# Performance work log

Hardware: AMD Instinct MI355X
Metric: run time of the kernel (lower is better)

The kernel has to match this reference:

```python
import jax, jax.numpy as jnp
import numpy as np

B, L, D, F = 1, 4096, 4096, 11008
# (start, end, side): side 0 = vision expert, side 1 = language expert.
# Mirrors merge_section_size over alternating contiguous vision/language token ranges.
SEGMENTS = [(0, 1024, 0), (1024, 2048, 1), (2048, 3072, 0), (3072, 4096, 1)]


def setup_inputs() -> dict:
    key = jax.random.key(0)
    ks = jax.random.split(key, 7)
    s = 0.02  # weight init scale
    hidden_states = jax.random.normal(ks[0], (B, L, D), jnp.float32)
    tt = np.zeros((B, L), np.int32)
    for a, b, side in SEGMENTS:
        tt[:, a:b] = side
    token_type_ids = jnp.asarray(tt)
    lg_w = jax.random.normal(ks[1], (D, F), jnp.float32) * s
    lu_w = jax.random.normal(ks[2], (D, F), jnp.float32) * s
    ld_w = jax.random.normal(ks[3], (F, D), jnp.float32) * s
    vg_w = jax.random.normal(ks[4], (D, F), jnp.float32) * s
    vu_w = jax.random.normal(ks[5], (D, F), jnp.float32) * s
    vd_w = jax.random.normal(ks[6], (F, D), jnp.float32) * s
    return {
        'hidden_states': hidden_states,
        'token_type_ids': token_type_ids,
        'lg_w': lg_w, 'lu_w': lu_w, 'ld_w': ld_w,
        'vg_w': vg_w, 'vu_w': vu_w, 'vd_w': vd_w,
    }


def _swiglu_mlp(x, gw, uw, dw):
    # x: [B, T, D] -> [B, T, D]; down(silu(gate(x)) * up(x))
    h = jax.nn.silu(jnp.einsum('btd,df->btf', x, gw)) * jnp.einsum('btd,df->btf', x, uw)
    return jnp.einsum('btf,fd->btd', h, dw)


def reference(hidden_states, token_type_ids, lg_w, lu_w, ld_w, vg_w, vu_w, vd_w):
    # Split-dispatch over static contiguous segments, then concat along seq dim.
    outs = []
    for a, b, side in SEGMENTS:
        seg = hidden_states[:, a:b, :]
        if side == 1:
            outs.append(_swiglu_mlp(seg, lg_w, lu_w, ld_w))
        else:
            outs.append(_swiglu_mlp(seg, vg_w, vu_w, vd_w))
    return jnp.concatenate(outs, axis=1)
```

## Files before the change

kernel.cpp:

```cpp
#include <hip/hip_runtime.h>
#include <math.h>

typedef unsigned short u16;
typedef short s16x8 __attribute__((ext_vector_type(8)));
typedef float f32x4 __attribute__((ext_vector_type(4)));

#define GLOAD16(gp, lp)                                                        \
  __builtin_amdgcn_global_load_lds(                                            \
      (const __attribute__((address_space(1))) void*)(gp),                     \
      (__attribute__((address_space(3))) void*)(lp), 16, 0, 0)

__device__ __forceinline__ u16 f2bf(float f) {
  union { float f; unsigned u; } v; v.f = f;
  unsigned r = v.u + 0x7fffu + ((v.u >> 16) & 1u);
  return (u16)(r >> 16);
}

__global__ __launch_bounds__(256) void cvt_x_kernel(const float* __restrict__ in,
                                                    u16* __restrict__ out) {
  size_t i = ((size_t)blockIdx.x * 256 + threadIdx.x) * 8;
  float4 a = *(const float4*)(in + i);
  float4 b = *(const float4*)(in + i + 4);
  s16x8 v;
  v[0] = (short)f2bf(a.x); v[1] = (short)f2bf(a.y);
  v[2] = (short)f2bf(a.z); v[3] = (short)f2bf(a.w);
  v[4] = (short)f2bf(b.x); v[5] = (short)f2bf(b.y);
  v[6] = (short)f2bf(b.z); v[7] = (short)f2bf(b.w);
  *(s16x8*)(out + i) = v;
}

__global__ __launch_bounds__(256) void transpose_cvt_kernel(
    const float* __restrict__ in0, const float* __restrict__ in1,
    const float* __restrict__ in2, const float* __restrict__ in3,
    const float* __restrict__ in4, const float* __restrict__ in5,
    u16* __restrict__ o01, u16* __restrict__ o23,
    u16* __restrict__ o4, u16* __restrict__ o5) {
  __shared__ float s[64 * 65];
  const int mat = blockIdx.y;
  const float* in; u16* out;
  switch (mat) {
    case 0: in = in0; out = o01; break;
    case 1: in = in1; out = o01; break;
    case 2: in = in2; out = o23; break;
    case 3: in = in3; out = o23; break;
    case 4: in = in4; out = o4; break;
    default: in = in5; out = o5; break;
  }
  const int R = (mat < 4) ? 4096 : 11008;
  const int C = (mat < 4) ? 11008 : 4096;
  const int nTc = C >> 6;
  const int tr = blockIdx.x / nTc, tc = blockIdx.x - tr * nTc;
  const int r0 = tr << 6, c0 = tc << 6;
  const int t = threadIdx.x;
#pragma unroll
  for (int p = 0; p < 4; ++p) {
    const int lr = p * 16 + (t >> 4);
    const int lc = (t & 15) * 4;
    float4 v = *(const float4*)(in + (size_t)(r0 + lr) * C + (c0 + lc));
    float* sp = &s[lr * 65 + lc];
    sp[0] = v.x; sp[1] = v.y; sp[2] = v.z; sp[3] = v.w;
  }
  __syncthreads();
#pragma unroll
  for (int q = 0; q < 2; ++q) {
    const int oc = q * 32 + (t >> 3);
    const int orr = (t & 7) * 8;
    s16x8 v;
#pragma unroll
    for (int i = 0; i < 8; ++i) v[i] = (short)f2bf(s[(orr + i) * 65 + oc]);
    const int f = c0 + oc;
    size_t orow;
    if (mat < 4) orow = (size_t)((f >> 4) << 5) + ((mat & 1) << 4) + (f & 15);
    else         orow = (size_t)f;
    *(s16x8*)(out + orow * R + (r0 + orr)) = v;
  }
}

template <int KB, int EPI>
__global__ __launch_bounds__(512, 1) void gemm256(
    const u16* __restrict__ A, const u16* __restrict__ Bl,
    const u16* __restrict__ Bv, const int* __restrict__ tt,
    void* __restrict__ OutP) {
  constexpr int NK = KB / 128;
  constexpr int L = NK / 2;
  __shared__ u16 sA[2][2][128][64];
  __shared__ u16 sB[2][2][128][64];

  const int nwg = gridDim.x;
  const int bid = blockIdx.x;
  const int wg = (bid & 7) * (nwg >> 3) + (bid >> 3);
  const int mT = wg & 15;
  const int nT = wg >> 4;

  const int t = threadIdx.x;
  const int lane = t & 63;
  const int rlo = lane & 15;
  const int hi = lane >> 4;
  const int wn = (t >> 6) & 3;
  const int wm = (t >> 8) & 1;

  const int side = tt[mT << 8];
  const u16* B = side ? Bl : Bv;

  const int rowq = t >> 3;
  const int gsw = ((t & 7) ^ (rowq & 7)) << 4;
  const char* srcA = (const char*)A + (size_t)(mT * 256 + rowq) * KB + gsw;
  const char* srcB = (const char*)B + (size_t)(nT * 256 + rowq) * KB + gsw;
  char* ldsA = (char*)&sA[0][0][0][0];
  char* ldsB = (char*)&sB[0][0][0][0];
  const int woff = (t & 448) << 4;

#define STG_A(d, h, kt)                                                        \
  do {                                                                         \
    GLOAD16(srcA + (size_t)((h) * 128) * KB + (kt) * 128,                      \
            ldsA + (d) * 32768 + (h) * 16384 + woff);                          \
    GLOAD16(srcA + (size_t)((h) * 128 + 64) * KB + (kt) * 128,                 \
            ldsA + (d) * 32768 + (h) * 16384 + 8192 + woff);                   \
  } while (0)
#define STG_B(d, h, kt)                                                        \
  do {                                                                         \
    GLOAD16(srcB + (size_t)((h) * 128) * KB + (kt) * 128,                      \
            ldsB + (d) * 32768 + (h) * 16384 + woff);                          \
    GLOAD16(srcB + (size_t)((h) * 128 + 64) * KB + (kt) * 128,                 \
            ldsB + (d) * 32768 + (h) * 16384 + 8192 + woff);                   \
  } while (0)

  const int cxa = (hi ^ (rlo & 7)) << 4;
  const int cxb = ((4 + hi) ^ (rlo & 7)) << 4;
  const int arow = (wm * 64 + rlo) * 128;
  const int brow = (wn * 32 + rlo) * 128;

  s16x8 af[4][2], bf[2][2];
  f32x4 acc[8][4];
  const f32x4 z = {0.f, 0.f, 0.f, 0.f};
#pragma unroll
  for (int i = 0; i < 8; ++i)
#pragma unroll
    for (int j = 0; j < 4; ++j) acc[i][j] = z;

#define LDA(d, mh)                                                             \
  do {                                                                         \
    _Pragma("unroll") for (int fi = 0; fi < 4; ++fi) {                         \
      const char* p = ldsA + (d) * 32768 + (mh) * 16384 + arow + fi * 2048;    \
      af[fi][0] = *(const s16x8*)(p + cxa);                                    \
      af[fi][1] = *(const s16x8*)(p + cxb);                                    \
    }                                                                          \
  } while (0)
#define LDB(d, nh)                                                             \
  do {                                                                         \
    _Pragma("unroll") for (int gi = 0; gi < 2; ++gi) {                         \
      const char* p = ldsB + (d) * 32768 + (nh) * 16384 + brow + gi * 2048;    \
      bf[gi][0] = *(const s16x8*)(p + cxa);                                    \
      bf[gi][1] = *(const s16x8*)(p + cxb);                                    \
    }                                                                          \
  } while (0)
#define MFMA16(mh, nh)                                                         \
  do {                                                                         \
    __builtin_amdgcn_s_setprio(1);                                             \
    _Pragma("unroll") for (int fi = 0; fi < 4; ++fi)                           \
        _Pragma("unroll") for (int gi = 0; gi < 2; ++gi) {                     \
      acc[(mh)*4 + fi][(nh)*2 + gi] = __builtin_amdgcn_mfma_f32_16x16x32_bf16( \
          af[fi][0], bf[gi][0], acc[(mh)*4 + fi][(nh)*2 + gi], 0, 0, 0);       \
      acc[(mh)*4 + fi][(nh)*2 + gi] = __builtin_amdgcn_mfma_f32_16x16x32_bf16( \
          af[fi][1], bf[gi][1], acc[(mh)*4 + fi][(nh)*2 + gi], 0, 0, 0);       \
    }                                                                          \
    __builtin_amdgcn_s_setprio(0);                                             \
  } while (0)
#define SBAR() __builtin_amdgcn_s_barrier()
#define VMCNT4() do { asm volatile("s_waitcnt vmcnt(4)" ::: "memory");         \
                      __builtin_amdgcn_sched_barrier(0); } while (0)
#define VMCNT0() do { asm volatile("s_waitcnt vmcnt(0)" ::: "memory");         \
                      __builtin_amdgcn_sched_barrier(0); } while (0)

  STG_A(0, 0, 0); STG_A(0, 1, 0); STG_B(0, 0, 0); STG_B(0, 1, 0);
  STG_B(1, 0, 1); STG_A(1, 1, 1);
  VMCNT4();
  SBAR();

  for (int it = 0; it < L - 1; ++it) {
    const int T = 2 * it;
    LDA(0, 0); LDB(0, 0);
    STG_A(1, 0, T + 1); STG_B(1, 1, T + 1);
    SBAR(); MFMA16(0, 0); SBAR();
    LDA(0, 1);
    SBAR(); MFMA16(1, 0); SBAR();
    LDB(0, 1);
    STG_B(0, 0, T + 2);
    SBAR(); MFMA16(1, 1); SBAR();
    LDA(0, 0);
    STG_A(0, 1, T + 2);
    SBAR(); MFMA16(0, 1);
    VMCNT4(); SBAR();
    LDA(1, 0); LDB(1, 0);
    STG_A(0, 0, T + 2); STG_B(0, 1, T + 2);
    SBAR(); MFMA16(0, 0); SBAR();
    LDA(1, 1);
    SBAR(); MFMA16(1, 0); SBAR();
    LDB(1, 1);
    STG_B(1, 0, T + 3);
    SBAR(); MFMA16(1, 1); SBAR();
    LDA(1, 0);
    STG_A(1, 1, T + 3);
    SBAR(); MFMA16(0, 1);
    VMCNT4(); SBAR();
  }
  {
    const int T = NK - 2;
    LDA(0, 0); LDB(0, 0);
    STG_A(1, 0, T + 1); STG_B(1, 1, T + 1);
    SBAR(); MFMA16(0, 0); SBAR();
    LDA(0, 1);
    SBAR(); MFMA16(1, 0); SBAR();
    LDB(0, 1);
    SBAR(); MFMA16(1, 1); SBAR();
    LDA(0, 0);
    SBAR(); MFMA16(0, 1);
    VMCNT0(); SBAR();
    LDA(1, 0); LDB(1, 0);
    SBAR(); MFMA16(0, 0); SBAR();
    LDA(1, 1);
    SBAR(); MFMA16(1, 0); SBAR();
    LDB(1, 1);
    SBAR(); MFMA16(1, 1); SBAR();
    LDA(1, 0);
    SBAR(); MFMA16(0, 1);
  }

  if (EPI == 0) {
    u16* H = (u16*)OutP;
#pragma unroll
    for (int mh = 0; mh < 2; ++mh)
#pragma unroll
      for (int fi = 0; fi < 4; ++fi) {
        const int row0 = mT * 256 + mh * 128 + wm * 64 + fi * 16 + hi * 4;
#pragma unroll
        for (int nh = 0; nh < 2; ++nh) {
          const int fc = nT * 128 + (nh * 4 + wn) * 16 + rlo;
          const f32x4 g = acc[mh * 4 + fi][nh * 2 + 0];
          const f32x4 u = acc[mh * 4 + fi][nh * 2 + 1];
#pragma unroll
          for (int r = 0; r < 4; ++r) {
            const float gv = g[r];
            const float hv = gv / (1.f + __expf(-gv)) * u[r];
            H[(size_t)(row0 + r) * 11008 + fc] = f2bf(hv);
          }
        }
      }
  } else {
    float* O = (float*)OutP;
#pragma unroll
    for (int mh = 0; mh < 2; ++mh)
#pragma unroll
      for (int fi = 0; fi < 4; ++fi) {
        const int row0 = mT * 256 + mh * 128 + wm * 64 + fi * 16 + hi * 4;
#pragma unroll
        for (int nh = 0; nh < 2; ++nh)
#pragma unroll
          for (int gi = 0; gi < 2; ++gi) {
            const int col = nT * 256 + nh * 128 + wn * 32 + gi * 16 + rlo;
            const f32x4 a = acc[mh * 4 + fi][nh * 2 + gi];
#pragma unroll
            for (int r = 0; r < 4; ++r)
              O[(size_t)(row0 + r) * 4096 + col] = a[r];
          }
      }
  }
#undef STG_A
#undef STG_B
#undef LDA
#undef LDB
#undef MFMA16
#undef SBAR
#undef VMCNT4
#undef VMCNT0
}

extern "C" void kernel_launch(void* const* d_in, const int* in_sizes, int n_in,
                              void* d_out, int out_size, void* d_ws, size_t ws_size,
                              hipStream_t stream) {
  (void)in_sizes; (void)n_in; (void)out_size; (void)ws_size;
  const float* x  = (const float*)d_in[0];
  const int*   tt = (const int*)d_in[1];
  const float* lg = (const float*)d_in[2];
  const float* lu = (const float*)d_in[3];
  const float* ld = (const float*)d_in[4];
  const float* vg = (const float*)d_in[5];
  const float* vu = (const float*)d_in[6];
  const float* vd = (const float*)d_in[7];

  u16* ws  = (u16*)d_ws;
  u16* xbf = ws;
  u16* GUl = xbf + 16777216;
  u16* GUv = GUl + 90177536;
  u16* ldT = GUv + 90177536;
  u16* vdT = ldT + 45088768;
  u16* hbuf = vdT + 45088768;

  cvt_x_kernel<<<dim3(8192), dim3(256), 0, stream>>>(x, xbf);
  transpose_cvt_kernel<<<dim3(11008, 6), dim3(256), 0, stream>>>(
      lg, lu, vg, vu, ld, vd, GUl, GUv, ldT, vdT);
  gemm256<8192, 0><<<dim3(1376), dim3(512), 0, stream>>>(xbf, GUl, GUv, tt, hbuf);
  gemm256<22016, 1><<<dim3(256), dim3(512), 0, stream>>>(hbuf, ldT, vdT, tt, d_out);
}
```

Baseline: 1.520 ms.

## Switch GEMMs to 32x32 MFMA, persistent atomic tile queue, new gate/up interleave

Both GEMMs move from 16x16x32 to 32x32x16 bf16 MFMA with a new fragment layout and a simpler single-buffer-step pipeline that uses lgkmcnt waits in place of extra barriers. The gate/up weight interleave changes from 16-row to 128-row blocks to match the new accumulator tiling. The gate/up GEMM becomes a persistent 256-block kernel pulling tiles from an atomic counter, which is reset with a memset each call. The aim is fewer LDS reads per MFMA, fewer barriers and better load balance, at the cost of an added atomic per tile and more register pressure from the wider accumulators.

```diff
diff --git a/kernel.cpp b/kernel.cpp
--- a/kernel.cpp
+++ b/kernel.cpp
@@ -4,6 +4,7 @@
 typedef unsigned short u16;
 typedef short s16x8 __attribute__((ext_vector_type(8)));
 typedef float f32x4 __attribute__((ext_vector_type(4)));
+typedef float f32x16 __attribute__((ext_vector_type(16)));
 
 #define GLOAD16(gp, lp)                                                        \
   __builtin_amdgcn_global_load_lds(                                            \
@@ -70,209 +71,259 @@
     for (int i = 0; i < 8; ++i) v[i] = (short)f2bf(s[(orr + i) * 65 + oc]);
     const int f = c0 + oc;
     size_t orow;
-    if (mat < 4) orow = (size_t)((f >> 4) << 5) + ((mat & 1) << 4) + (f & 15);
+    if (mat < 4) orow = (size_t)((f >> 7) << 8) + ((mat & 1) << 7) + (f & 127);
     else         orow = (size_t)f;
     *(s16x8*)(out + orow * R + (r0 + orr)) = v;
   }
 }
 
-template <int KB, int EPI>
-__global__ __launch_bounds__(512, 1) void gemm256(
-    const u16* __restrict__ A, const u16* __restrict__ Bl,
-    const u16* __restrict__ Bv, const int* __restrict__ tt,
-    void* __restrict__ OutP) {
-  constexpr int NK = KB / 128;
-  constexpr int L = NK / 2;
+#define SBAR() __builtin_amdgcn_s_barrier()
+#define LGKM0() asm volatile("s_waitcnt lgkmcnt(0)")
+#define VMCNT4() asm volatile("s_waitcnt vmcnt(4)")
+#define VMCNT2() asm volatile("s_waitcnt vmcnt(2)")
+#define VMCNT0() asm volatile("s_waitcnt vmcnt(0)")
+
+#define LDA(d, mh)                                                             \
+  do {                                                                         \
+    _Pragma("unroll") for (int fj = 0; fj < 2; ++fj)                           \
+        _Pragma("unroll") for (int ks = 0; ks < 4; ++ks)                       \
+        af[fj][ks] = *(const s16x8*)(ldsA + (d) * 32768 + (mh) * 16384 +       \
+                                     arow + fj * 4096 + cx[ks]);               \
+  } while (0)
+#define LDB(d, nh)                                                             \
+  do {                                                                         \
+    _Pragma("unroll") for (int ks = 0; ks < 4; ++ks)                           \
+        bf[nh][ks] = *(const s16x8*)(ldsB + (d) * 32768 + (nh) * 16384 +       \
+                                     brow + cx[ks]);                           \
+  } while (0)
+#define MFMA8(mh, nh)                                                          \
+  do {                                                                         \
+    __builtin_amdgcn_s_setprio(1);                                             \
+    _Pragma("unroll") for (int fj = 0; fj < 2; ++fj)                           \
+        _Pragma("unroll") for (int ks = 0; ks < 4; ++ks)                       \
+        acc[mh][fj][nh] = __builtin_amdgcn_mfma_f32_32x32x16_bf16(             \
+            af[fj][ks], bf[nh][ks], acc[mh][fj][nh], 0, 0, 0);                 \
+    __builtin_amdgcn_s_setprio(0);                                             \
+  } while (0)
+
+#define STG_A(d, h, kt)                                                        \
+  do {                                                                         \
+    GLOAD16(srcA + (size_t)((h) * 128) * KB + (size_t)(kt) * 128,              \
+            ldsA + (d) * 32768 + (h) * 16384 + woff);                          \
+    GLOAD16(srcA + (size_t)((h) * 128 + 64) * KB + (size_t)(kt) * 128,         \
+            ldsA + (d) * 32768 + (h) * 16384 + 8192 + woff);                   \
+  } while (0)
+#define STG_B(d, h, kt)                                                        \
+  do {                                                                         \
+    GLOAD16(srcB + (size_t)((h) * 128) * KB + (size_t)(kt) * 128,              \
+            ldsB + (d) * 32768 + (h) * 16384 + woff);                          \
+    GLOAD16(srcB + (size_t)((h) * 128 + 64) * KB + (size_t)(kt) * 128,         \
+            ldsB + (d) * 32768 + (h) * 16384 + 8192 + woff);                   \
+  } while (0)
+
+__global__ __launch_bounds__(512, 1) void gemm_gateup_persist(
+    const u16* __restrict__ A, const u16* __restrict__ GUl,
+    const u16* __restrict__ GUv, const int* __restrict__ tt,
+    u16* __restrict__ H, int* __restrict__ qcnt) {
+  constexpr int KB = 8192;
+  constexpr int NKT = 64;
   __shared__ u16 sA[2][2][128][64];
   __shared__ u16 sB[2][2][128][64];
-
-  const int nwg = gridDim.x;
+  __shared__ int sQ;
+
+  const int t = threadIdx.x;
+  const int lane = t & 63;
+  const int l31 = lane & 31;
+  const int kg = lane >> 5;
+  const int wn = (t >> 6) & 3;
+  const int wm = (t >> 8) & 1;
+
+  const int rowq = t >> 3;
+  const int gsw = ((t & 7) ^ (rowq & 7)) << 4;
+  char* ldsA = (char*)&sA[0][0][0][0];
+  char* ldsB = (char*)&sB[0][0][0][0];
+  const int woff = (t & 448) << 4;
+
+  const int arow = (wm * 64 + l31) * 128;
+  const int brow = (wn * 32 + l31) * 128;
+  int cx[4];
+#pragma unroll
+  for (int ks = 0; ks < 4; ++ks) cx[ks] = ((2 * ks + kg) ^ (lane & 7)) << 4;
+
+  for (;;) {
+    __syncthreads();
+    if (t == 0) sQ = atomicAdd(qcnt, 1);
+    __syncthreads();
+    const int q = sQ;
+    if (q >= 1376) break;
+    const int nT = q >> 4;
+    const int mT = q & 15;
+    const int side = tt[mT << 8];
+    const u16* GU = side ? GUl : GUv;
+    const char* srcA = (const char*)A + (size_t)(mT * 256 + rowq) * KB + gsw;
+    const char* srcB = (const char*)GU + (size_t)(nT * 256 + rowq) * KB + gsw;
+
+    s16x8 af[2][4], bf[2][4];
+    f32x16 acc[2][2][2];
+#pragma unroll
+    for (int a = 0; a < 2; ++a)
+#pragma unroll
+      for (int b = 0; b < 2; ++b)
+#pragma unroll
+        for (int c = 0; c < 2; ++c)
+#pragma unroll
+          for (int r = 0; r < 16; ++r) acc[a][b][c][r] = 0.f;
+
+    STG_A(0, 0, 0); STG_B(0, 0, 0); STG_B(0, 1, 0); STG_A(0, 1, 0);
+    VMCNT4();
+    SBAR();
+
+    for (int T = 0; T < NKT - 1; ++T) {
+      const int d = T & 1, nd = d ^ 1;
+      LDA(d, 0); LDB(d, 0);
+      STG_A(nd, 0, T + 1);
+      LGKM0(); MFMA8(0, 0);
+      VMCNT4(); SBAR();
+      LDB(d, 1);
+      STG_B(nd, 0, T + 1);
+      LGKM0(); MFMA8(0, 1);
+      VMCNT4(); SBAR();
+      LDA(d, 1);
+      STG_B(nd, 1, T + 1);
+      LGKM0(); MFMA8(1, 1);
+      STG_A(nd, 1, T + 1);
+      MFMA8(1, 0);
+      VMCNT4(); SBAR();
+    }
+    {
+      const int d = (NKT - 1) & 1;
+      LDA(d, 0); LDB(d, 0);
+      LGKM0(); MFMA8(0, 0);
+      VMCNT2(); SBAR();
+      LDB(d, 1);
+      LGKM0(); MFMA8(0, 1);
+      VMCNT0(); SBAR();
+      LDA(d, 1);
+      LGKM0(); MFMA8(1, 1);
+      MFMA8(1, 0);
+    }
+
+    const int f = nT * 128 + wn * 32 + l31;
+#pragma unroll
+    for (int mh = 0; mh < 2; ++mh)
+#pragma unroll
+      for (int fj = 0; fj < 2; ++fj) {
+        const int rowbase = mT * 256 + mh * 128 + wm * 64 + fj * 32 + 4 * kg;
+#pragma unroll
+        for (int r = 0; r < 16; ++r) {
+          const int row = rowbase + (r & 3) + 8 * (r >> 2);
+          const float gv = acc[mh][fj][0][r];
+          const float uv = acc[mh][fj][1][r];
+          const float hv = gv / (1.f + __expf(-gv)) * uv;
+          H[(size_t)row * 11008 + f] = f2bf(hv);
+        }
+      }
+  }
+}
+
+__global__ __launch_bounds__(512, 1) void gemm_down(
+    const u16* __restrict__ Hm, const u16* __restrict__ Dl,
+    const u16* __restrict__ Dv, const int* __restrict__ tt,
+    float* __restrict__ O) {
+  constexpr int KB = 22016;
+  constexpr int NKT = 172;
+  __shared__ u16 sA[2][2][128][64];
+  __shared__ u16 sB[2][2][128][64];
+
   const int bid = blockIdx.x;
-  const int wg = (bid & 7) * (nwg >> 3) + (bid >> 3);
+  const int wg = (bid & 7) * 32 + (bid >> 3);
   const int mT = wg & 15;
   const int nT = wg >> 4;
 
   const int t = threadIdx.x;
   const int lane = t & 63;
-  const int rlo = lane & 15;
-  const int hi = lane >> 4;
+  const int l31 = lane & 31;
+  const int kg = lane >> 5;
   const int wn = (t >> 6) & 3;
   const int wm = (t >> 8) & 1;
 
   const int side = tt[mT << 8];
-  const u16* B = side ? Bl : Bv;
+  const u16* B = side ? Dl : Dv;
 
   const int rowq = t >> 3;
   const int gsw = ((t & 7) ^ (rowq & 7)) << 4;
-  const char* srcA = (const char*)A + (size_t)(mT * 256 + rowq) * KB + gsw;
+  const char* srcA = (const char*)Hm + (size_t)(mT * 256 + rowq) * KB + gsw;
   const char* srcB = (const char*)B + (size_t)(nT * 256 + rowq) * KB + gsw;
   char* ldsA = (char*)&sA[0][0][0][0];
   char* ldsB = (char*)&sB[0][0][0][0];
   const int woff = (t & 448) << 4;
 
-#define STG_A(d, h, kt)                                                        \
-  do {                                                                         \
-    GLOAD16(srcA + (size_t)((h) * 128) * KB + (kt) * 128,                      \
-            ldsA + (d) * 32768 + (h) * 16384 + woff);                          \
-    GLOAD16(srcA + (size_t)((h) * 128 + 64) * KB + (kt) * 128,                 \
-            ldsA + (d) * 32768 + (h) * 16384 + 8192 + woff);                   \
-  } while (0)
-#define STG_B(d, h, kt)                                                        \
-  do {                                                                         \
-    GLOAD16(srcB + (size_t)((h) * 128) * KB + (kt) * 128,                      \
-            ldsB + (d) * 32768 + (h) * 16384 + woff);                          \
-    GLOAD16(srcB + (size_t)((h) * 128 + 64) * KB + (kt) * 128,                 \
-            ldsB + (d) * 32768 + (h) * 16384 + 8192 + woff);                   \
-  } while (0)
-
-  const int cxa = (hi ^ (rlo & 7)) << 4;
-  const int cxb = ((4 + hi) ^ (rlo & 7)) << 4;
-  const int arow = (wm * 64 + rlo) * 128;
-  const int brow = (wn * 32 + rlo) * 128;
-
-  s16x8 af[4][2], bf[2][2];
-  f32x4 acc[8][4];
-  const f32x4 z = {0.f, 0.f, 0.f, 0.f};
-#pragma unroll
-  for (int i = 0; i < 8; ++i)
-#pragma unroll
-    for (int j = 0; j < 4; ++j) acc[i][j] = z;
-
-#define LDA(d, mh)                                                             \
-  do {                                                                         \
-    _Pragma("unroll") for (int fi = 0; fi < 4; ++fi) {                         \
-      const char* p = ldsA + (d) * 32768 + (mh) * 16384 + arow + fi * 2048;    \
-      af[fi][0] = *(const s16x8*)(p + cxa);                                    \
-      af[fi][1] = *(const s16x8*)(p + cxb);                                    \
-    }                                                                          \
-  } while (0)
-#define LDB(d, nh)                                                             \
-  do {                                                                         \
-    _Pragma("unroll") for (int gi = 0; gi < 2; ++gi) {                         \
-      const char* p = ldsB + (d) * 32768 + (nh) * 16384 + brow + gi * 2048;    \
-      bf[gi][0] = *(const s16x8*)(p + cxa);                                    \
-      bf[gi][1] = *(const s16x8*)(p + cxb);                                    \
-    }                                                                          \
-  } while (0)
-#define MFMA16(mh, nh)                                                         \
-  do {                                                                         \
-    __builtin_amdgcn_s_setprio(1);                                             \
-    _Pragma("unroll") for (int fi = 0; fi < 4; ++fi)                           \
-        _Pragma("unroll") for (int gi = 0; gi < 2; ++gi) {                     \
-      acc[(mh)*4 + fi][(nh)*2 + gi] = __builtin_amdgcn_mfma_f32_16x16x32_bf16( \
-          af[fi][0], bf[gi][0], acc[(mh)*4 + fi][(nh)*2 + gi], 0, 0, 0);       \
-      acc[(mh)*4 + fi][(nh)*2 + gi] = __builtin_amdgcn_mfma_f32_16x16x32_bf16( \
-          af[fi][1], bf[gi][1], acc[(mh)*4 + fi][(nh)*2 + gi], 0, 0, 0);       \
-    }                                                                          \
-    __builtin_amdgcn_s_setprio(0);                                             \
-  } while (0)
-#define SBAR() __builtin_amdgcn_s_barrier()
-#define VMCNT4() do { asm volatile("s_waitcnt vmcnt(4)" ::: "memory");         \
-                      __builtin_amdgcn_sched_barrier(0); } while (0)
-#define VMCNT0() do { asm volatile("s_waitcnt vmcnt(0)" ::: "memory");         \
-                      __builtin_amdgcn_sched_barrier(0); } while (0)
-
-  STG_A(0, 0, 0); STG_A(0, 1, 0); STG_B(0, 0, 0); STG_B(0, 1, 0);
-  STG_B(1, 0, 1); STG_A(1, 1, 1);
+  const int arow = (wm * 64 + l31) * 128;
+  const int brow = (wn * 32 + l31) * 128;
+  int cx[4];
+#pragma unroll
+  for (int ks = 0; ks < 4; ++ks) cx[ks] = ((2 * ks + kg) ^ (lane & 7)) << 4;
+
+  s16x8 af[2][4], bf[2][4];
+  f32x16 acc[2][2][2];
+#pragma unroll
+  for (int a = 0; a < 2; ++a)
+#pragma unroll
+    for (int b = 0; b < 2; ++b)
+#pragma unroll
+      for (int c = 0; c < 2; ++c)
+#pragma unroll
+        for (int r = 0; r < 16; ++r) acc[a][b][c][r] = 0.f;
+
+  STG_A(0, 0, 0); STG_B(0, 0, 0); STG_B(0, 1, 0); STG_A(0, 1, 0);
   VMCNT4();
   SBAR();
 
-  for (int it = 0; it < L - 1; ++it) {
-    const int T = 2 * it;
-    LDA(0, 0); LDB(0, 0);
-    STG_A(1, 0, T + 1); STG_B(1, 1, T + 1);
-    SBAR(); MFMA16(0, 0); SBAR();
-    LDA(0, 1);
-    SBAR(); MFMA16(1, 0); SBAR();
-    LDB(0, 1);
-    STG_B(0, 0, T + 2);
-    SBAR(); MFMA16(1, 1); SBAR();
-    LDA(0, 0);
-    STG_A(0, 1, T + 2);
-    SBAR(); MFMA16(0, 1);
+  for (int T = 0; T < NKT - 1; ++T) {
+    const int d = T & 1, nd = d ^ 1;
+    LDA(d, 0); LDB(d, 0);
+    STG_A(nd, 0, T + 1);
+    LGKM0(); MFMA8(0, 0);
     VMCNT4(); SBAR();
-    LDA(1, 0); LDB(1, 0);
-    STG_A(0, 0, T + 2); STG_B(0, 1, T + 2);
-    SBAR(); MFMA16(0, 0); SBAR();
-    LDA(1, 1);
-    SBAR(); MFMA16(1, 0); SBAR();
-    LDB(1, 1);
-    STG_B(1, 0, T + 3);
-    SBAR(); MFMA16(1, 1); SBAR();
-    LDA(1, 0);
-    STG_A(1, 1, T + 3);
-    SBAR(); MFMA16(0, 1);
+    LDB(d, 1);
+    STG_B(nd, 0, T + 1);
+    LGKM0(); MFMA8(0, 1);
     VMCNT4(); SBAR();
+    LDA(d, 1);
+    STG_B(nd, 1, T + 1);
+    LGKM0(); MFMA8(1, 1);
+    STG_A(nd, 1, T + 1);
+    MFMA8(1, 0);
+    VMCNT4(); SBAR();
   }
   {
-    const int T = NK - 2;
-    LDA(0, 0); LDB(0, 0);
-    STG_A(1, 0, T + 1); STG_B(1, 1, T + 1);
-    SBAR(); MFMA16(0, 0); SBAR();
-    LDA(0, 1);
-    SBAR(); MFMA16(1, 0); SBAR();
-    LDB(0, 1);
-    SBAR(); MFMA16(1, 1); SBAR();
-    LDA(0, 0);
-    SBAR(); MFMA16(0, 1);
+    const int d = (NKT - 1) & 1;
+    LDA(d, 0); LDB(d, 0);
+    LGKM0(); MFMA8(0, 0);
+    VMCNT2(); SBAR();
+    LDB(d, 1);
+    LGKM0(); MFMA8(0, 1);
     VMCNT0(); SBAR();
-    LDA(1, 0); LDB(1, 0);
-    SBAR(); MFMA16(0, 0); SBAR();
-    LDA(1, 1);
-    SBAR(); MFMA16(1, 0); SBAR();
-    LDB(1, 1);
-    SBAR(); MFMA16(1, 1); SBAR();
-    LDA(1, 0);
-    SBAR(); MFMA16(0, 1);
-  }
-
-  if (EPI == 0) {
-    u16* H = (u16*)OutP;
-#pragma unroll
-    for (int mh = 0; mh < 2; ++mh)
-#pragma unroll
-      for (int fi = 0; fi < 4; ++fi) {
-        const int row0 = mT * 256 + mh * 128 + wm * 64 + fi * 16 + hi * 4;
-#pragma unroll
-        for (int nh = 0; nh < 2; ++nh) {
-          const int fc = nT * 128 + (nh * 4 + wn) * 16 + rlo;
-          const f32x4 g = acc[mh * 4 + fi][nh * 2 + 0];
-          const f32x4 u = acc[mh * 4 + fi][nh * 2 + 1];
-#pragma unroll
-          for (int r = 0; r < 4; ++r) {
-            const float gv = g[r];
-            const float hv = gv / (1.f + __expf(-gv)) * u[r];
-            H[(size_t)(row0 + r) * 11008 + fc] = f2bf(hv);
-          }
+    LDA(d, 1);
+    LGKM0(); MFMA8(1, 1);
+    MFMA8(1, 0);
+  }
+
+#pragma unroll
+  for (int mh = 0; mh < 2; ++mh)
+#pragma unroll
+    for (int fj = 0; fj < 2; ++fj) {
+      const int rowbase = mT * 256 + mh * 128 + wm * 64 + fj * 32 + 4 * kg;
+#pragma unroll
+      for (int nh = 0; nh < 2; ++nh) {
+        const int col = nT * 256 + nh * 128 + wn * 32 + l31;
+#pragma unroll
+        for (int r = 0; r < 16; ++r) {
+          const int row = rowbase + (r & 3) + 8 * (r >> 2);
+          O[(size_t)row * 4096 + col] = acc[mh][fj][nh][r];
         }
       }
-  } else {
-    float* O = (float*)OutP;
-#pragma unroll
-    for (int mh = 0; mh < 2; ++mh)
-#pragma unroll
-      for (int fi = 0; fi < 4; ++fi) {
-        const int row0 = mT * 256 + mh * 128 + wm * 64 + fi * 16 + hi * 4;
-#pragma unroll
-        for (int nh = 0; nh < 2; ++nh)
-#pragma unroll
-          for (int gi = 0; gi < 2; ++gi) {
-            const int col = nT * 256 + nh * 128 + wn * 32 + gi * 16 + rlo;
-            const f32x4 a = acc[mh * 4 + fi][nh * 2 + gi];
-#pragma unroll
-            for (int r = 0; r < 4; ++r)
-              O[(size_t)(row0 + r) * 4096 + col] = a[r];
-          }
-      }
-  }
-#undef STG_A
-#undef STG_B
-#undef LDA
-#undef LDB
-#undef MFMA16
-#undef SBAR
-#undef VMCNT4
-#undef VMCNT0
+    }
 }
 
 extern "C" void kernel_launch(void* const* d_in, const int* in_sizes, int n_in,
@@ -295,10 +346,13 @@
   u16* ldT = GUv + 90177536;
   u16* vdT = ldT + 45088768;
   u16* hbuf = vdT + 45088768;
-
+  int* qcnt = (int*)(hbuf + 45088768);
+
+  hipMemsetAsync(qcnt, 0, 4, stream);
   cvt_x_kernel<<<dim3(8192), dim3(256), 0, stream>>>(x, xbf);
   transpose_cvt_kernel<<<dim3(11008, 6), dim3(256), 0, stream>>>(
       lg, lu, vg, vu, ld, vd, GUl, GUv, ldT, vdT);
-  gemm256<8192, 0><<<dim3(1376), dim3(512), 0, stream>>>(xbf, GUl, GUv, tt, hbuf);
-  gemm256<22016, 1><<<dim3(256), dim3(512), 0, stream>>>(hbuf, ldT, vdT, tt, d_out);
-}
+  gemm_gateup_persist<<<dim3(256), dim3(512), 0, stream>>>(
+      xbf, GUl, GUv, tt, hbuf, qcnt);
+  gemm_down<<<dim3(256), dim3(512), 0, stream>>>(hbuf, ldT, vdT, tt, (float*)d_out);
+}
```

New measurement: 1.410 ms. 1.08x faster.
